# Optimization experiments

Measured on AMD Instinct MI355X. Metric: run time of the kernel, lower is better.

## Reference

```python
import jax, jax.numpy as jnp
import numpy as np

B, S, DIN, DH = 8, 8192, 256, 256


def setup_inputs() -> dict:
    key = jax.random.key(0)
    k0, k1, k2, k3, k4 = jax.random.split(key, 5)
    stdv = 1.0 / np.sqrt(DIN)
    x = jax.random.normal(k0, (B, S, DIN), jnp.float32)
    W0 = jax.random.uniform(k1, (2 * DH, DIN), jnp.float32, -stdv, stdv)
    b0 = jax.random.uniform(k2, (2 * DH,), jnp.float32, -stdv, stdv)
    stdv2 = 1.0 / np.sqrt(DH)
    W1 = jax.random.uniform(k3, (2 * DH, DH), jnp.float32, -stdv2, stdv2)
    b1 = jax.random.uniform(k4, (2 * DH,), jnp.float32, -stdv2, stdv2)
    return {"x": x, "W0": W0, "b0": b0, "W1": W1, "b1": b1}


def _log_g(x):
    # log of g(x) = x + 0.5 for x >= 0 else sigmoid(x)
    return jnp.where(x >= 0, jnp.log(jax.nn.relu(x) + 0.5), -jax.nn.softplus(-x))


def _mingru_layer(x, W, b):
    # x: (B,S,Din); W: (2*DH, Din); b: (2*DH,)
    gh = jnp.einsum('bsd,ed->bse', x, W) + b          # (B,S,2*DH)
    gate, hidden = jnp.split(gh, 2, axis=-1)          # each (B,S,DH)
    log_coeffs = -jax.nn.softplus(gate)               # log(1 - z)
    log_vals = -jax.nn.softplus(-gate) + _log_g(hidden)  # log z + log h_tilde
    Bb, Ss, Dd = log_coeffs.shape
    # initial hidden h0 = g(0) = 0.5  ->  log(h0) = log(0.5)
    log_h0 = jnp.full((Bb, 1, Dd), jnp.log(0.5), log_coeffs.dtype)
    log_values = jnp.concatenate([log_h0, log_vals], axis=1)          # (B,S+1,DH)
    a_star = jnp.concatenate(
        [jnp.zeros((Bb, 1, Dd), log_coeffs.dtype), jnp.cumsum(log_coeffs, axis=1)],
        axis=1)                                                       # (B,S+1,DH)
    log_h = a_star + jax.lax.cumlogsumexp(log_values - a_star, axis=1)
    return jnp.exp(log_h)[:, 1:]                                      # (B,S,DH)


def reference(x, W0, b0, W1, b1):
    out0 = _mingru_layer(x, W0, b0)
    out1 = _mingru_layer(out0, W1, b1)
    h = jnp.stack([out0[:, -1:], out1[:, -1:]])  # (num_layers,B,1,DH)
    return out1, h
```

## Files before the change

### kernel.cpp

```cpp
#include <hip/hip_runtime.h>
#include <hip/hip_bf16.h>

#define Bb 8
#define Ss 8192
#define Dd 256
#define Mm (Bb * Ss)
#define Nn 512
#define NCHUNK 128
#define CLEN (Ss / NCHUNK)

typedef __hip_bfloat16 bf16;
typedef __attribute__((ext_vector_type(8))) short short8;
typedef __attribute__((ext_vector_type(4))) float f32x4;

__device__ __forceinline__ void load_lds16(const void* g, void* l) {
  __builtin_amdgcn_global_load_lds(
      (const __attribute__((address_space(1))) void*)g,
      (__attribute__((address_space(3))) void*)l, 16, 0, 0);
}

__global__ __launch_bounds__(256) void cvt_f32_bf16(const float* __restrict__ in,
                                                    bf16* __restrict__ out,
                                                    long n4) {
  long i = (long)blockIdx.x * blockDim.x + threadIdx.x;
  if (i >= n4) return;
  const float4 v = ((const float4*)in)[i];
  union { ushort4 u; bf16 h[4]; } o;
  o.h[0] = __float2bfloat16(v.x);
  o.h[1] = __float2bfloat16(v.y);
  o.h[2] = __float2bfloat16(v.z);
  o.h[3] = __float2bfloat16(v.w);
  ((ushort4*)out)[i] = o.u;
}

__device__ __forceinline__ void av_from_gh(float gate, float hid, float& a,
                                           float& v) {
  gate = fminf(fmaxf(gate, -20.f), 20.f);
  float eg = __expf(gate);
  a = 1.f / (1.f + eg);
  float z = eg * a;
  float gfun;
  if (hid >= 0.f) {
    gfun = hid + 0.5f;
  } else {
    float eh = __expf(fmaxf(hid, -20.f));
    gfun = eh / (1.f + eh);
  }
  v = z * gfun;
}

__device__ __forceinline__ unsigned pack_av(float a, float v) {
  union { bf16 h[2]; unsigned u; } o;
  o.h[0] = __float2bfloat16(a);
  o.h[1] = __float2bfloat16(v);
  return o.u;
}

__global__ __launch_bounds__(256) void gemm_av(const bf16* __restrict__ X,
                                               const bf16* __restrict__ W,
                                               const float* __restrict__ bias,
                                               unsigned* __restrict__ AV) {
  __shared__ __align__(16) bf16 As[128 * 32];
  __shared__ __align__(16) bf16 Bs[128 * 32];

  const int tid = threadIdx.x;
  const int w = tid >> 6;
  const int l = tid & 63;
  const int fl = l & 15;
  const int q = l >> 4;

  const long rowBase = (long)blockIdx.x * 128;
  const int cb = blockIdx.y;

  const int wrow = (w >> 1) * 64;
  const int wc = (w & 1) * 32;

  const int sr = tid >> 2;
  const int sc = (tid & 3) * 8;

  f32x4 acc[4][4];
#pragma unroll
  for (int i = 0; i < 4; i++)
#pragma unroll
    for (int j = 0; j < 4; j++) acc[i][j] = (f32x4)0.0f;

  for (int k0 = 0; k0 < 256; k0 += 32) {
    __syncthreads();
    load_lds16(X + (rowBase + sr) * 256 + k0 + sc, &As[(long)w * 512]);
    load_lds16(X + (rowBase + 64 + sr) * 256 + k0 + sc, &As[2048 + (long)w * 512]);
    load_lds16(W + (cb * 64 + sr) * 256 + k0 + sc, &Bs[(long)w * 512]);
    load_lds16(W + (256 + cb * 64 + sr) * 256 + k0 + sc, &Bs[2048 + (long)w * 512]);
    __syncthreads();

    short8 af[4], bfr[4];
#pragma unroll
    for (int mt = 0; mt < 4; mt++)
      af[mt] = *(const short8*)&As[(wrow + 16 * mt + fl) * 32 + q * 8];
#pragma unroll
    for (int nt = 0; nt < 4; nt++) {
      const int brow = (nt < 2) ? (wc + 16 * nt + fl) : (64 + wc + 16 * (nt - 2) + fl);
      bfr[nt] = *(const short8*)&Bs[brow * 32 + q * 8];
    }

#pragma unroll
    for (int mt = 0; mt < 4; mt++)
#pragma unroll
      for (int nt = 0; nt < 4; nt++)
        acc[mt][nt] = __builtin_amdgcn_mfma_f32_16x16x32_bf16(
            af[mt], bfr[nt], acc[mt][nt], 0, 0, 0);
  }

  float bg[2], bh[2];
#pragma unroll
  for (int p = 0; p < 2; p++) {
    const int d = cb * 64 + wc + 16 * p + fl;
    bg[p] = bias[d];
    bh[p] = bias[256 + d];
  }
#pragma unroll
  for (int mt = 0; mt < 4; mt++) {
#pragma unroll
    for (int p = 0; p < 2; p++) {
      const int d = cb * 64 + wc + 16 * p + fl;
      const long r0 = rowBase + wrow + 16 * mt + q * 4;
#pragma unroll
      for (int r = 0; r < 4; r++) {
        float a, v;
        av_from_gh(acc[mt][p][r] + bg[p], acc[mt][p + 2][r] + bh[p], a, v);
        AV[(r0 + r) * 256 + d] = pack_av(a, v);
      }
    }
  }
}

__global__ __launch_bounds__(256) void scan_partial(
    const unsigned* __restrict__ AV, float* __restrict__ Asum,
    float* __restrict__ Vsum) {
  const int d = threadIdx.x;
  const int c = blockIdx.x % NCHUNK;
  const int b = blockIdx.x / NCHUNK;
  float A = 1.f, H = 0.f;
  long base = ((long)b * Ss + (long)c * CLEN) * 256 + d;
#pragma unroll 8
  for (int t = 0; t < CLEN; t++) {
    const unsigned p = AV[base];
    const float a = __uint_as_float((p & 0xffffu) << 16);
    const float v = __uint_as_float(p & 0xffff0000u);
    A *= a;
    H = a * H + v;
    base += 256;
  }
  Asum[(long)blockIdx.x * 256 + d] = A;
  Vsum[(long)blockIdx.x * 256 + d] = H;
}

__global__ __launch_bounds__(256) void scan_combine(
    const float* __restrict__ Asum, const float* __restrict__ Vsum,
    float* __restrict__ Hin) {
  const int d = threadIdx.x;
  const int b = blockIdx.x;
  float h = 0.5f;
#pragma unroll 8
  for (int c = 0; c < NCHUNK; c++) {
    const long i = ((long)b * NCHUNK + c) * 256 + d;
    Hin[i] = h;
    h = Asum[i] * h + Vsum[i];
  }
}

template <bool WRITE_BF16>
__global__ __launch_bounds__(256) void scan_final(
    const unsigned* __restrict__ AV, const float* __restrict__ Hin,
    bf16* __restrict__ OutB, float* __restrict__ OutF,
    float* __restrict__ Hlast) {
  const int d = threadIdx.x;
  const int c = blockIdx.x % NCHUNK;
  const int b = blockIdx.x / NCHUNK;
  float h = Hin[(long)blockIdx.x * 256 + d];
  long base = ((long)b * Ss + (long)c * CLEN) * 256 + d;
#pragma unroll 8
  for (int t = 0; t < CLEN; t++) {
    const unsigned p = AV[base];
    const float a = __uint_as_float((p & 0xffffu) << 16);
    const float v = __uint_as_float(p & 0xffff0000u);
    h = a * h + v;
    if (WRITE_BF16)
      OutB[base] = __float2bfloat16(h);
    else
      OutF[base] = h;
    base += 256;
  }
  if (c == NCHUNK - 1) Hlast[b * 256 + d] = h;
}

extern "C" void kernel_launch(void* const* d_in, const int* in_sizes, int n_in,
                              void* d_out, int out_size, void* d_ws,
                              size_t ws_size, hipStream_t stream) {
  const float* x = (const float*)d_in[0];
  const float* W0f = (const float*)d_in[1];
  const float* b0 = (const float*)d_in[2];
  const float* W1f = (const float*)d_in[3];
  const float* b1 = (const float*)d_in[4];

  float* outF = (float*)d_out;
  float* hlast = outF + (long)Mm * 256;
  bf16* Xb = (bf16*)d_out;

  char* ws = (char*)d_ws;
  unsigned* AV = (unsigned*)ws;
  bf16* W0b = (bf16*)(ws + (long)Mm * 256 * 4);
  bf16* W1b = W0b + (long)Nn * Dd;
  float* Asum = (float*)(W1b + (long)Nn * Dd);
  float* Vsum = Asum + (long)Bb * NCHUNK * 256;
  float* Hin = Vsum + (long)Bb * NCHUNK * 256;

  const dim3 gemmGrid(Mm / 128, 4);
  const dim3 blk(256);
  const dim3 scanGrid(Bb * NCHUNK);

  {
    const long n4x = (long)Mm * Dd / 4;
    cvt_f32_bf16<<<dim3((n4x + 255) / 256), blk, 0, stream>>>(x, Xb, n4x);
    const long n4w = (long)Nn * Dd / 4;
    cvt_f32_bf16<<<dim3((n4w + 255) / 256), blk, 0, stream>>>(W0f, W0b, n4w);
    cvt_f32_bf16<<<dim3((n4w + 255) / 256), blk, 0, stream>>>(W1f, W1b, n4w);
  }

  gemm_av<<<gemmGrid, blk, 0, stream>>>(Xb, W0b, b0, AV);
  scan_partial<<<scanGrid, blk, 0, stream>>>(AV, Asum, Vsum);
  scan_combine<<<dim3(Bb), blk, 0, stream>>>(Asum, Vsum, Hin);
  scan_final<true><<<scanGrid, blk, 0, stream>>>(AV, Hin, Xb, nullptr, hlast);

  gemm_av<<<gemmGrid, blk, 0, stream>>>(Xb, W1b, b1, AV);
  scan_partial<<<scanGrid, blk, 0, stream>>>(AV, Asum, Vsum);
  scan_combine<<<dim3(Bb), blk, 0, stream>>>(Asum, Vsum, Hin);
  scan_final<false><<<scanGrid, blk, 0, stream>>>(AV, Hin, nullptr, outF,
                                                  hlast + Bb * 256);
}
```

Before: 279.8 us.

## Fuse fp32-to-bf16 input conversion into GEMM and load fragments directly from global

Removes the separate conversion pass over x by letting the first-layer GEMM read fp32 rows and convert them to bf16 in registers. Replaces the LDS staging in the GEMM with direct per-lane global fragment loads and no block barriers. Swaps the grid axes so the four column blocks sharing an A tile are adjacent and can hit in cache. The risk is that each wave now reads A fragments from global memory, with redundant reads across the two column-wave groups, and the fragment loads are uncoalesced strided accesses.

```diff
diff --git a/kernel.cpp b/kernel.cpp
--- a/kernel.cpp
+++ b/kernel.cpp
@@ -12,12 +12,6 @@
 typedef __hip_bfloat16 bf16;
 typedef __attribute__((ext_vector_type(8))) short short8;
 typedef __attribute__((ext_vector_type(4))) float f32x4;
-
-__device__ __forceinline__ void load_lds16(const void* g, void* l) {
-  __builtin_amdgcn_global_load_lds(
-      (const __attribute__((address_space(1))) void*)g,
-      (__attribute__((address_space(3))) void*)l, 16, 0, 0);
-}
 
 __global__ __launch_bounds__(256) void cvt_f32_bf16(const float* __restrict__ in,
                                                     bf16* __restrict__ out,
@@ -56,27 +50,41 @@
   return o.u;
 }
 
-__global__ __launch_bounds__(256) void gemm_av(const bf16* __restrict__ X,
+__device__ __forceinline__ short8 ld_frag_bf16(const bf16* p) {
+  return *(const short8*)p;
+}
+__device__ __forceinline__ short8 ld_frag_f32(const float* p) {
+  const float4 a = ((const float4*)p)[0];
+  const float4 b = ((const float4*)p)[1];
+  const float vals[8] = {a.x, a.y, a.z, a.w, b.x, b.y, b.z, b.w};
+  short8 r;
+#pragma unroll
+  for (int i = 0; i < 8; i++) {
+    union { bf16 h; short s; } t;
+    t.h = __float2bfloat16(vals[i]);
+    r[i] = t.s;
+  }
+  return r;
+}
+
+template <bool F32A>
+__global__ __launch_bounds__(256) void gemm_av(const void* __restrict__ Xv,
                                                const bf16* __restrict__ W,
                                                const float* __restrict__ bias,
                                                unsigned* __restrict__ AV) {
-  __shared__ __align__(16) bf16 As[128 * 32];
-  __shared__ __align__(16) bf16 Bs[128 * 32];
-
   const int tid = threadIdx.x;
   const int w = tid >> 6;
   const int l = tid & 63;
   const int fl = l & 15;
   const int q = l >> 4;
 
-  const long rowBase = (long)blockIdx.x * 128;
-  const int cb = blockIdx.y;
+  const int cb = blockIdx.x;
+  const long rowBase = (long)blockIdx.y * 128;
 
   const int wrow = (w >> 1) * 64;
   const int wc = (w & 1) * 32;
 
-  const int sr = tid >> 2;
-  const int sc = (tid & 3) * 8;
+  const bf16* Bg = W + (long)(cb * 64 + wc + fl) * 256 + q * 8;
 
   f32x4 acc[4][4];
 #pragma unroll
@@ -84,23 +92,23 @@
 #pragma unroll
     for (int j = 0; j < 4; j++) acc[i][j] = (f32x4)0.0f;
 
-  for (int k0 = 0; k0 < 256; k0 += 32) {
-    __syncthreads();
-    load_lds16(X + (rowBase + sr) * 256 + k0 + sc, &As[(long)w * 512]);
-    load_lds16(X + (rowBase + 64 + sr) * 256 + k0 + sc, &As[2048 + (long)w * 512]);
-    load_lds16(W + (cb * 64 + sr) * 256 + k0 + sc, &Bs[(long)w * 512]);
-    load_lds16(W + (256 + cb * 64 + sr) * 256 + k0 + sc, &Bs[2048 + (long)w * 512]);
-    __syncthreads();
-
+  const long arow = (rowBase + wrow + fl) * 256 + q * 8;
+
+#pragma unroll
+  for (int ks = 0; ks < 8; ks++) {
+    const int k0 = ks * 32;
     short8 af[4], bfr[4];
 #pragma unroll
-    for (int mt = 0; mt < 4; mt++)
-      af[mt] = *(const short8*)&As[(wrow + 16 * mt + fl) * 32 + q * 8];
-#pragma unroll
-    for (int nt = 0; nt < 4; nt++) {
-      const int brow = (nt < 2) ? (wc + 16 * nt + fl) : (64 + wc + 16 * (nt - 2) + fl);
-      bfr[nt] = *(const short8*)&Bs[brow * 32 + q * 8];
+    for (int mt = 0; mt < 4; mt++) {
+      if (F32A)
+        af[mt] = ld_frag_f32((const float*)Xv + arow + (long)mt * 16 * 256 + k0);
+      else
+        af[mt] = ld_frag_bf16((const bf16*)Xv + arow + (long)mt * 16 * 256 + k0);
     }
+    bfr[0] = ld_frag_bf16(Bg + k0);
+    bfr[1] = ld_frag_bf16(Bg + 16 * 256 + k0);
+    bfr[2] = ld_frag_bf16(Bg + 256 * 256 + k0);
+    bfr[3] = ld_frag_bf16(Bg + (256 + 16) * 256 + k0);
 
 #pragma unroll
     for (int mt = 0; mt < 4; mt++)
@@ -214,24 +222,22 @@
   float* Vsum = Asum + (long)Bb * NCHUNK * 256;
   float* Hin = Vsum + (long)Bb * NCHUNK * 256;
 
-  const dim3 gemmGrid(Mm / 128, 4);
+  const dim3 gemmGrid(4, Mm / 128);
   const dim3 blk(256);
   const dim3 scanGrid(Bb * NCHUNK);
 
   {
-    const long n4x = (long)Mm * Dd / 4;
-    cvt_f32_bf16<<<dim3((n4x + 255) / 256), blk, 0, stream>>>(x, Xb, n4x);
     const long n4w = (long)Nn * Dd / 4;
     cvt_f32_bf16<<<dim3((n4w + 255) / 256), blk, 0, stream>>>(W0f, W0b, n4w);
     cvt_f32_bf16<<<dim3((n4w + 255) / 256), blk, 0, stream>>>(W1f, W1b, n4w);
   }
 
-  gemm_av<<<gemmGrid, blk, 0, stream>>>(Xb, W0b, b0, AV);
+  gemm_av<true><<<gemmGrid, blk, 0, stream>>>(x, W0b, b0, AV);
   scan_partial<<<scanGrid, blk, 0, stream>>>(AV, Asum, Vsum);
   scan_combine<<<dim3(Bb), blk, 0, stream>>>(Asum, Vsum, Hin);
   scan_final<true><<<scanGrid, blk, 0, stream>>>(AV, Hin, Xb, nullptr, hlast);
 
-  gemm_av<<<gemmGrid, blk, 0, stream>>>(Xb, W1b, b1, AV);
+  gemm_av<false><<<gemmGrid, blk, 0, stream>>>(Xb, W1b, b1, AV);
   scan_partial<<<scanGrid, blk, 0, stream>>>(AV, Asum, Vsum);
   scan_combine<<<dim3(Bb), blk, 0, stream>>>(Asum, Vsum, Hin);
   scan_final<false><<<scanGrid, blk, 0, stream>>>(AV, Hin, nullptr, outF,
```

New measurement: 358.9 us. +28.3%, slower.
